# Kernel optimization log

Hardware: AMD Instinct MI355X
Metric: run time of the kernel (lower is better)

Reference implementation:

```python
import jax, jax.numpy as jnp
import numpy as np

DIM = 768
NUM_HEADS = 12
HEAD_DIM = DIM // NUM_HEADS
SCALE = HEAD_DIM ** -0.5
B, N = 4, 2048


def setup_inputs() -> dict:
    key = jax.random.key(0)
    k1, k2, k3 = jax.random.split(key, 3)
    x = jax.random.normal(k1, (B, N, DIM), dtype=jnp.float32)
    W_qk = jax.random.normal(k2, (2 * DIM, DIM), dtype=jnp.float32) * (DIM ** -0.5)
    b_qk = jax.random.normal(k3, (2 * DIM,), dtype=jnp.float32) * 0.02
    return {"x": x, "W_qk": W_qk, "b_qk": b_qk}


def reference(x, W_qk, b_qk):
    Bb, Nn, C = x.shape
    # qk projection: [B,N,2C] -> [B,N,2,H,D] -> q,k each [B,H,N,D]
    qk = x @ W_qk.T + b_qk
    qk = qk.reshape(Bb, Nn, 2, NUM_HEADS, HEAD_DIM).transpose(2, 0, 3, 1, 4)
    q, k = qk[0], qk[1]
    # attention scores [B,H,N,N]
    attn = jnp.einsum("bhnd,bhmd->bhnm", q, k) * SCALE
    attn = jax.nn.softmax(attn, axis=-1)
    # mean over heads, then per-query diagonal -> [B,N]
    attn_weights = jnp.diagonal(attn.mean(axis=1), axis1=-2, axis2=-1)
    return attn_weights
```

## Files before the change

kernel.cpp:

```cpp
#include <hip/hip_runtime.h>
#include <math.h>


#define B_ 4
#define N_ 2048
#define H_ 12
#define D_ 64
#define C_ 768
#define TWO_C 1536
#define QSCALE 0.18033688011112043f

typedef _Float16 half8 __attribute__((ext_vector_type(8)));
typedef _Float16 half4 __attribute__((ext_vector_type(4)));
typedef float floatx4 __attribute__((ext_vector_type(4)));

#if __has_builtin(__builtin_amdgcn_exp2f)
#define EXP2(x) __builtin_amdgcn_exp2f(x)
#else
#define EXP2(x) exp2f(x)
#endif

__device__ __forceinline__ void gload_lds16(const _Float16* g, _Float16* l) {
  __builtin_amdgcn_global_load_lds(
      (const __attribute__((address_space(1))) void*)g,
      (__attribute__((address_space(3))) void*)l, 16, 0, 0);
}

#define NX4 1572864
#define NW4 294912
__global__ __launch_bounds__(256) void conv_kernel(const float* __restrict__ x,
                                                   const float* __restrict__ W,
                                                   _Float16* __restrict__ xh,
                                                   _Float16* __restrict__ wh) {
  int i = blockIdx.x * 256 + threadIdx.x;
  const float* in;
  _Float16* out;
  int idx;
  if (i < NX4) {
    in = x; out = xh; idx = i;
  } else if (i < NX4 + NW4) {
    in = W; out = wh; idx = i - NX4;
  } else {
    return;
  }
  float4 v = ((const float4*)in)[idx];
  half4 o;
  o[0] = (_Float16)v.x; o[1] = (_Float16)v.y;
  o[2] = (_Float16)v.z; o[3] = (_Float16)v.w;
  ((half4*)out)[idx] = o;
}

__global__ __launch_bounds__(256) void proj_kernel(
    const _Float16* __restrict__ xh, const _Float16* __restrict__ wh,
    const float* __restrict__ bias, _Float16* __restrict__ qh,
    _Float16* __restrict__ kh) {
  __shared__ _Float16 As[3][128 * 32];
  __shared__ _Float16 Bs[3][128 * 32];
  const int t = threadIdx.x;
  const int l = t & 63;
  const int w = t >> 6;
  const int wr = w >> 1, wc = w & 1;

  int lin = blockIdx.y * 12 + blockIdx.x;
  int swz = (lin & 7) * 96 + (lin >> 3);
  const int bm = (swz / 12) * 128;
  const int bc = (swz % 12) * 128;

  const int srow = l >> 2;
  const int schunk = (l & 3) ^ ((l >> 3) & 3);

  floatx4 acc[4][4] = {};

#define PSTAGE(KT)                                                          \
  {                                                                         \
    const int sl_ = (KT) % 3;                                               \
    const int k0_ = (KT) * 32;                                              \
    _Pragma("unroll") for (int i_ = 0; i_ < 2; ++i_) {                      \
      int rb_ = w * 32 + i_ * 16;                                           \
      gload_lds16(xh + (size_t)(bm + rb_ + srow) * C_ + k0_ + schunk * 8,   \
                  As[sl_] + rb_ * 32);                                      \
      gload_lds16(wh + (size_t)(bc + rb_ + srow) * C_ + k0_ + schunk * 8,   \
                  Bs[sl_] + rb_ * 32);                                      \
    }                                                                       \
  }

#define PITER(KT, VMASM, DO_STAGE)                                          \
  {                                                                         \
    asm volatile(VMASM ::: "memory");                                       \
    __builtin_amdgcn_s_barrier();                                           \
    asm volatile("" ::: "memory");                                          \
    const int sl_ = (KT) % 3;                                               \
    const _Float16* Ap_ = As[sl_];                                          \
    const _Float16* Bp_ = Bs[sl_];                                          \
    half8 af[4], bf[4];                                                     \
    _Pragma("unroll") for (int fr = 0; fr < 4; ++fr) {                      \
      int row = wr * 64 + fr * 16 + (l & 15);                               \
      int ch = (l >> 4) ^ ((row >> 1) & 3);                                 \
      af[fr] = *(const half8*)(Ap_ + row * 32 + ch * 8);                    \
    }                                                                       \
    _Pragma("unroll") for (int fc = 0; fc < 4; ++fc) {                      \
      int row = wc * 64 + fc * 16 + (l & 15);                               \
      int ch = (l >> 4) ^ ((row >> 1) & 3);                                 \
      bf[fc] = *(const half8*)(Bp_ + row * 32 + ch * 8);                    \
    }                                                                       \
    if (DO_STAGE) PSTAGE((KT) + 2);                                         \
    _Pragma("unroll") for (int fr = 0; fr < 4; ++fr)                        \
        _Pragma("unroll") for (int fc = 0; fc < 4; ++fc) acc[fr][fc] =      \
        __builtin_amdgcn_mfma_f32_16x16x32_f16(af[fr], bf[fc],              \
                                               acc[fr][fc], 0, 0, 0);       \
  }

  PSTAGE(0);
  PSTAGE(1);
  for (int kt = 0; kt < 22; ++kt) PITER(kt, "s_waitcnt vmcnt(4)", true);
  PITER(22, "s_waitcnt vmcnt(4)", false);
  PITER(23, "s_waitcnt vmcnt(0)", false);
#undef PITER
#undef PSTAGE

#pragma unroll
  for (int fr = 0; fr < 4; ++fr) {
#pragma unroll
    for (int fc = 0; fc < 4; ++fc) {
#pragma unroll
      for (int j = 0; j < 4; ++j) {
        int m = bm + wr * 64 + fr * 16 + ((l >> 4) << 2) + j;
        int c = bc + wc * 64 + fc * 16 + (l & 15);
        float v = acc[fr][fc][j] + bias[c];
        int b = m >> 11, n = m & (N_ - 1);
        int cc = (c < C_) ? c : c - C_;
        if (c < C_) v *= QSCALE;
        int hh = cc >> 6, d = cc & 63;
        _Float16* dst = (c < C_) ? qh : kh;
        dst[((((size_t)b * H_ + hh) * N_ + n) << 6) + d] = (_Float16)v;
      }
    }
  }
}

__global__ __launch_bounds__(256) void attn_kernel(
    const _Float16* __restrict__ qh, const _Float16* __restrict__ kh,
    float* __restrict__ part) {
  __shared__ _Float16 ks[4][64 * 64];
  const int t = threadIdx.x;
  const int l = t & 63;
  const int w = t >> 6;

  int lin = blockIdx.x;
  int swz = (lin & 7) * 192 + (lin >> 3);
  const int qt = swz & 31;
  const int h = (swz >> 5) % 12;
  const int b = swz / 384;

  const _Float16* qb = qh + (((size_t)(b * H_ + h) * N_ + qt * 64) << 6);
  const _Float16* kb = kh + (((size_t)(b * H_ + h) * N_) << 6);

  half8 qf[4][2];
#pragma unroll
  for (int fr = 0; fr < 4; ++fr)
#pragma unroll
    for (int kd = 0; kd < 2; ++kd)
      qf[fr][kd] = *(const half8*)(qb + (size_t)(fr * 16 + (l & 15)) * 64 +
                                   kd * 32 + (l >> 4) * 8);

  const int lin0 = w * 64 + l;
  const int row0 = lin0 >> 3, slot0 = lin0 & 7;
  const int soff0 = row0 * 64 + (slot0 ^ (row0 & 7)) * 8;
  const int lin1 = lin0 + 256;
  const int row1 = lin1 >> 3, slot1 = lin1 & 7;
  const int soff1 = row1 * 64 + (slot1 ^ (row1 & 7)) * 8;

#define STAGE(KT)                                                   \
  {                                                                 \
    const _Float16* kp_ = kb + (size_t)(KT) * 4096;                 \
    _Float16* ld_ = ks[(KT) & 3];                                   \
    gload_lds16(kp_ + soff0, ld_ + w * 512);                        \
    gload_lds16(kp_ + soff1, ld_ + w * 512 + 2048);                 \
  }

  const int frow = w * 16 + (l & 15);
  const int koff0 = frow * 64 + (((l >> 4) + 0) ^ (l & 7)) * 8;
  const int koff1 = frow * 64 + (((l >> 4) + 4) ^ (l & 7)) * 8;

  float lsum[4][4] = {};
  float ed[4] = {0.f, 0.f, 0.f, 0.f};
  const floatx4 kZero = {0.f, 0.f, 0.f, 0.f};
  floatx4 accA[4], accB[4];

#define FINB(KT, ACC)                                                         \
  {                                                                           \
    _Pragma("unroll") for (int fr = 0; fr < 4; ++fr)                          \
        _Pragma("unroll") for (int j = 0; j < 4; ++j)                         \
            lsum[fr][j] += EXP2(ACC[fr][j]);                                  \
    if ((KT) == qt) {                                                         \
      _Pragma("unroll") for (int fr = 0; fr < 4; ++fr)                        \
          _Pragma("unroll") for (int j = 0; j < 4; ++j) {                     \
        if (fr == w && (l & 15) == (((l >> 4) << 2) + j))                     \
          ed[j] = EXP2(ACC[fr][j]);                                           \
      }                                                                       \
    }                                                                         \
  }

#define STEP(KT, ACCC, ACCP, VMASM, DO_STAGE, DO_FIN)                         \
  {                                                                           \
    asm volatile(VMASM ::: "memory");                                         \
    __builtin_amdgcn_s_barrier();                                             \
    asm volatile("" ::: "memory");                                            \
    const _Float16* bufp = ks[(KT) & 3];                                      \
    half8 kf0 = *(const half8*)(bufp + koff0);                                \
    half8 kf1 = *(const half8*)(bufp + koff1);                                \
    if (DO_STAGE) STAGE((KT) + 3);                                            \
    if (DO_FIN) FINB((KT) - 1, ACCP);                                         \
    _Pragma("unroll") for (int fr = 0; fr < 4; ++fr) {                        \
      ACCC[fr] = kZero;                                                       \
      ACCC[fr] = __builtin_amdgcn_mfma_f32_16x16x32_f16(qf[fr][0], kf0,       \
                                                        ACCC[fr], 0, 0, 0);   \
      ACCC[fr] = __builtin_amdgcn_mfma_f32_16x16x32_f16(qf[fr][1], kf1,       \
                                                        ACCC[fr], 0, 0, 0);   \
    }                                                                         \
  }

  STAGE(0);
  STAGE(1);
  STAGE(2);

  STEP(0, accA, accB, "s_waitcnt vmcnt(4)", true, false);
  for (int kt = 1; kt < 28; kt += 2) {
    STEP(kt, accB, accA, "s_waitcnt vmcnt(4)", true, true);
    STEP(kt + 1, accA, accB, "s_waitcnt vmcnt(4)", true, true);
  }
  STEP(29, accB, accA, "s_waitcnt vmcnt(4)", false, true);
  STEP(30, accA, accB, "s_waitcnt vmcnt(2)", false, true);
  STEP(31, accB, accA, "s_waitcnt vmcnt(0)", false, true);
  FINB(31, accB);
#undef STEP
#undef FINB
#undef STAGE

#pragma unroll
  for (int fr = 0; fr < 4; ++fr)
#pragma unroll
    for (int j = 0; j < 4; ++j)
#pragma unroll
      for (int m = 1; m < 16; m <<= 1)
        lsum[fr][j] += __shfl_xor(lsum[fr][j], m, 16);
#pragma unroll
  for (int j = 0; j < 4; ++j)
#pragma unroll
    for (int m = 1; m < 16; m <<= 1) ed[j] += __shfl_xor(ed[j], m, 16);

  __builtin_amdgcn_s_barrier();
  float* red = (float*)ks[0];
  float* edl = red + 256;
  if ((l & 15) == 0) {
#pragma unroll
    for (int fr = 0; fr < 4; ++fr)
#pragma unroll
      for (int j = 0; j < 4; ++j)
        red[w * 64 + fr * 16 + ((l >> 4) << 2) + j] = lsum[fr][j];
#pragma unroll
    for (int j = 0; j < 4; ++j) edl[w * 16 + ((l >> 4) << 2) + j] = ed[j];
  }
  __syncthreads();

  if (t < 64) {
    float ls = red[t] + red[64 + t] + red[128 + t] + red[192 + t];
    part[(size_t)(b * H_ + h) * N_ + qt * 64 + t] = edl[t] / ls;
  }
}

__global__ __launch_bounds__(256) void reduce_kernel(
    const float* __restrict__ part, float* __restrict__ out) {
  int g = blockIdx.x * 256 + threadIdx.x;
  if (g >= B_ * N_) return;
  int b = g >> 11, n = g & (N_ - 1);
  float s = 0.0f;
#pragma unroll
  for (int hh = 0; hh < H_; ++hh) s += part[(size_t)(b * H_ + hh) * N_ + n];
  out[g] = s * (1.0f / (float)H_);
}

extern "C" void kernel_launch(void* const* d_in, const int* in_sizes, int n_in,
                              void* d_out, int out_size, void* d_ws,
                              size_t ws_size, hipStream_t stream) {
  const float* x = (const float*)d_in[0];
  const float* W = (const float*)d_in[1];
  const float* bias = (const float*)d_in[2];
  float* out = (float*)d_out;

  char* ws = (char*)d_ws;
  _Float16* xh = (_Float16*)ws;
  _Float16* wh = (_Float16*)(ws + 12582912);
  _Float16* qh = (_Float16*)(ws + 14942208);
  _Float16* kh = (_Float16*)(ws + 27525120);
  float* part = (float*)(ws + 40108032);

  conv_kernel<<<(NX4 + NW4 + 255) / 256, 256, 0, stream>>>(x, W, xh, wh);
  proj_kernel<<<dim3(TWO_C / 128, 8192 / 128), 256, 0, stream>>>(xh, wh, bias,
                                                                 qh, kh);
  attn_kernel<<<N_ / 64 * H_ * B_, 256, 0, stream>>>(qh, kh, part);
  reduce_kernel<<<(B_ * N_ + 255) / 256, 256, 0, stream>>>(part, out);
}
```

Baseline: 84.45 us.

## Double query tile per block to 128 rows and drop accumulator double-buffering

Each attention block now processes 128 query rows (8 MFMA fragments) instead of 64, so every staged K tile in LDS is reused across twice as many queries and total K traffic halves. The grid shrinks to 768 blocks. The software-pipelined accA/accB ping-pong that overlapped exp with the next tile's MFMAs is replaced by a single accumulator computed and exponentiated in the same iteration. This costs more registers, which may lower occupancy, and leaves less overlap between MFMA and exp work.

Result: no change. 84.91 us (+0.5%).

```diff
diff --git a/kernel.cpp b/kernel.cpp
--- a/kernel.cpp
+++ b/kernel.cpp
@@ -147,17 +147,17 @@
   const int w = t >> 6;
 
   int lin = blockIdx.x;
-  int swz = (lin & 7) * 192 + (lin >> 3);
-  const int qt = swz & 31;
-  const int h = (swz >> 5) % 12;
-  const int b = swz / 384;
-
-  const _Float16* qb = qh + (((size_t)(b * H_ + h) * N_ + qt * 64) << 6);
+  int swz = (lin & 7) * 96 + (lin >> 3);
+  const int qt = swz & 15;
+  const int h = (swz >> 4) % 12;
+  const int b = swz / 192;
+
+  const _Float16* qb = qh + (((size_t)(b * H_ + h) * N_ + qt * 128) << 6);
   const _Float16* kb = kh + (((size_t)(b * H_ + h) * N_) << 6);
 
-  half8 qf[4][2];
-#pragma unroll
-  for (int fr = 0; fr < 4; ++fr)
+  half8 qf[8][2];
+#pragma unroll
+  for (int fr = 0; fr < 8; ++fr)
 #pragma unroll
     for (int kd = 0; kd < 2; ++kd)
       qf[fr][kd] = *(const half8*)(qb + (size_t)(fr * 16 + (l & 15)) * 64 +
@@ -182,26 +182,15 @@
   const int koff0 = frow * 64 + (((l >> 4) + 0) ^ (l & 7)) * 8;
   const int koff1 = frow * 64 + (((l >> 4) + 4) ^ (l & 7)) * 8;
 
-  float lsum[4][4] = {};
-  float ed[4] = {0.f, 0.f, 0.f, 0.f};
-  const floatx4 kZero = {0.f, 0.f, 0.f, 0.f};
-  floatx4 accA[4], accB[4];
-
-#define FINB(KT, ACC)                                                         \
-  {                                                                           \
-    _Pragma("unroll") for (int fr = 0; fr < 4; ++fr)                          \
-        _Pragma("unroll") for (int j = 0; j < 4; ++j)                         \
-            lsum[fr][j] += EXP2(ACC[fr][j]);                                  \
-    if ((KT) == qt) {                                                         \
-      _Pragma("unroll") for (int fr = 0; fr < 4; ++fr)                        \
-          _Pragma("unroll") for (int j = 0; j < 4; ++j) {                     \
-        if (fr == w && (l & 15) == (((l >> 4) << 2) + j))                     \
-          ed[j] = EXP2(ACC[fr][j]);                                           \
-      }                                                                       \
-    }                                                                         \
-  }
-
-#define STEP(KT, ACCC, ACCP, VMASM, DO_STAGE, DO_FIN)                         \
+  float lsum[8][4] = {};
+  float ed0[4] = {0.f, 0.f, 0.f, 0.f};
+  float ed1[4] = {0.f, 0.f, 0.f, 0.f};
+
+  STAGE(0);
+  STAGE(1);
+  STAGE(2);
+
+#define ITER(KT, VMASM, DO_STAGE)                                             \
   {                                                                           \
     asm volatile(VMASM ::: "memory");                                         \
     __builtin_amdgcn_s_barrier();                                             \
@@ -210,35 +199,41 @@
     half8 kf0 = *(const half8*)(bufp + koff0);                                \
     half8 kf1 = *(const half8*)(bufp + koff1);                                \
     if (DO_STAGE) STAGE((KT) + 3);                                            \
-    if (DO_FIN) FINB((KT) - 1, ACCP);                                         \
-    _Pragma("unroll") for (int fr = 0; fr < 4; ++fr) {                        \
-      ACCC[fr] = kZero;                                                       \
-      ACCC[fr] = __builtin_amdgcn_mfma_f32_16x16x32_f16(qf[fr][0], kf0,       \
-                                                        ACCC[fr], 0, 0, 0);   \
-      ACCC[fr] = __builtin_amdgcn_mfma_f32_16x16x32_f16(qf[fr][1], kf1,       \
-                                                        ACCC[fr], 0, 0, 0);   \
+    floatx4 acc[8] = {};                                                      \
+    _Pragma("unroll") for (int fr = 0; fr < 8; ++fr) {                        \
+      acc[fr] = __builtin_amdgcn_mfma_f32_16x16x32_f16(qf[fr][0], kf0,        \
+                                                       acc[fr], 0, 0, 0);     \
+      acc[fr] = __builtin_amdgcn_mfma_f32_16x16x32_f16(qf[fr][1], kf1,        \
+                                                       acc[fr], 0, 0, 0);     \
     }                                                                         \
-  }
-
-  STAGE(0);
-  STAGE(1);
-  STAGE(2);
-
-  STEP(0, accA, accB, "s_waitcnt vmcnt(4)", true, false);
-  for (int kt = 1; kt < 28; kt += 2) {
-    STEP(kt, accB, accA, "s_waitcnt vmcnt(4)", true, true);
-    STEP(kt + 1, accA, accB, "s_waitcnt vmcnt(4)", true, true);
-  }
-  STEP(29, accB, accA, "s_waitcnt vmcnt(4)", false, true);
-  STEP(30, accA, accB, "s_waitcnt vmcnt(2)", false, true);
-  STEP(31, accB, accA, "s_waitcnt vmcnt(0)", false, true);
-  FINB(31, accB);
-#undef STEP
-#undef FINB
+    _Pragma("unroll") for (int fr = 0; fr < 8; ++fr)                          \
+        _Pragma("unroll") for (int j = 0; j < 4; ++j)                         \
+            lsum[fr][j] += EXP2(acc[fr][j]);                                  \
+    if ((KT) == 2 * qt) {                                                     \
+      _Pragma("unroll") for (int fr = 0; fr < 8; ++fr)                        \
+          _Pragma("unroll") for (int j = 0; j < 4; ++j) {                     \
+        if (fr == w && (l & 15) == (((l >> 4) << 2) + j))                     \
+          ed0[j] = EXP2(acc[fr][j]);                                          \
+      }                                                                       \
+    }                                                                         \
+    if ((KT) == 2 * qt + 1) {                                                 \
+      _Pragma("unroll") for (int fr = 0; fr < 8; ++fr)                        \
+          _Pragma("unroll") for (int j = 0; j < 4; ++j) {                     \
+        if (fr == w + 4 && (l & 15) == (((l >> 4) << 2) + j))                 \
+          ed1[j] = EXP2(acc[fr][j]);                                          \
+      }                                                                       \
+    }                                                                         \
+  }
+
+  for (int kt = 0; kt < 29; ++kt) ITER(kt, "s_waitcnt vmcnt(4)", true);
+  ITER(29, "s_waitcnt vmcnt(4)", false);
+  ITER(30, "s_waitcnt vmcnt(2)", false);
+  ITER(31, "s_waitcnt vmcnt(0)", false);
+#undef ITER
 #undef STAGE
 
 #pragma unroll
-  for (int fr = 0; fr < 4; ++fr)
+  for (int fr = 0; fr < 8; ++fr)
 #pragma unroll
     for (int j = 0; j < 4; ++j)
 #pragma unroll
@@ -247,25 +242,31 @@
 #pragma unroll
   for (int j = 0; j < 4; ++j)
 #pragma unroll
-    for (int m = 1; m < 16; m <<= 1) ed[j] += __shfl_xor(ed[j], m, 16);
+    for (int m = 1; m < 16; m <<= 1) {
+      ed0[j] += __shfl_xor(ed0[j], m, 16);
+      ed1[j] += __shfl_xor(ed1[j], m, 16);
+    }
 
   __builtin_amdgcn_s_barrier();
   float* red = (float*)ks[0];
-  float* edl = red + 256;
+  float* edl = red + 512;
   if ((l & 15) == 0) {
 #pragma unroll
-    for (int fr = 0; fr < 4; ++fr)
+    for (int fr = 0; fr < 8; ++fr)
 #pragma unroll
       for (int j = 0; j < 4; ++j)
-        red[w * 64 + fr * 16 + ((l >> 4) << 2) + j] = lsum[fr][j];
-#pragma unroll
-    for (int j = 0; j < 4; ++j) edl[w * 16 + ((l >> 4) << 2) + j] = ed[j];
+        red[w * 128 + fr * 16 + ((l >> 4) << 2) + j] = lsum[fr][j];
+#pragma unroll
+    for (int j = 0; j < 4; ++j) {
+      edl[w * 16 + ((l >> 4) << 2) + j] = ed0[j];
+      edl[64 + w * 16 + ((l >> 4) << 2) + j] = ed1[j];
+    }
   }
   __syncthreads();
 
-  if (t < 64) {
-    float ls = red[t] + red[64 + t] + red[128 + t] + red[192 + t];
-    part[(size_t)(b * H_ + h) * N_ + qt * 64 + t] = edl[t] / ls;
+  if (t < 128) {
+    float ls = red[t] + red[128 + t] + red[256 + t] + red[384 + t];
+    part[(size_t)(b * H_ + h) * N_ + qt * 128 + t] = edl[t] / ls;
   }
 }
 
@@ -298,6 +299,6 @@
   conv_kernel<<<(NX4 + NW4 + 255) / 256, 256, 0, stream>>>(x, W, xh, wh);
   proj_kernel<<<dim3(TWO_C / 128, 8192 / 128), 256, 0, stream>>>(xh, wh, bias,
                                                                  qh, kh);
-  attn_kernel<<<N_ / 64 * H_ * B_, 256, 0, stream>>>(qh, kh, part);
+  attn_kernel<<<N_ / 128 * H_ * B_, 256, 0, stream>>>(qh, kh, part);
   reduce_kernel<<<(B_ * N_ + 255) / 256, 256, 0, stream>>>(part, out);
 }
```

## Process K tiles in pairs and fuse head reduction via atomics

Applied to the files above, without the earlier changes.

The attention loop now stages and consumes two 64-key tiles per iteration, using a 3-slot buffer of 128-key pairs in place of a 4-slot ring of single tiles. Both accumulator sets are computed and their exponentials summed in the same iteration, which halves the number of barriers. The separate reduce kernel is removed: the output is zeroed inside the conversion kernel and each attention block adds its head's contribution with atomicAdd. This saves one launch and the round trip through the partial buffer, at the cost of atomic contention and a summation order that is no longer deterministic.

Measured after the change: 126.9 us. 50.2% more time.

```diff
diff --git a/kernel.cpp b/kernel.cpp
--- a/kernel.cpp
+++ b/kernel.cpp
@@ -31,8 +31,13 @@
 __global__ __launch_bounds__(256) void conv_kernel(const float* __restrict__ x,
                                                    const float* __restrict__ W,
                                                    _Float16* __restrict__ xh,
-                                                   _Float16* __restrict__ wh) {
+                                                   _Float16* __restrict__ wh,
+                                                   float* __restrict__ outz) {
   int i = blockIdx.x * 256 + threadIdx.x;
+  if (i < 2048) {
+    float4 z; z.x = 0.f; z.y = 0.f; z.z = 0.f; z.w = 0.f;
+    ((float4*)outz)[i] = z;
+  }
   const float* in;
   _Float16* out;
   int idx;
@@ -140,8 +145,8 @@
 
 __global__ __launch_bounds__(256) void attn_kernel(
     const _Float16* __restrict__ qh, const _Float16* __restrict__ kh,
-    float* __restrict__ part) {
-  __shared__ _Float16 ks[4][64 * 64];
+    float* __restrict__ out) {
+  __shared__ _Float16 ks[3 * 8192];
   const int t = threadIdx.x;
   const int l = t & 63;
   const int w = t >> 6;
@@ -170,12 +175,14 @@
   const int row1 = lin1 >> 3, slot1 = lin1 & 7;
   const int soff1 = row1 * 64 + (slot1 ^ (row1 & 7)) * 8;
 
-#define STAGE(KT)                                                   \
+#define SPAIR(PM, SLOT)                                             \
   {                                                                 \
-    const _Float16* kp_ = kb + (size_t)(KT) * 4096;                 \
-    _Float16* ld_ = ks[(KT) & 3];                                   \
+    const _Float16* kp_ = kb + (size_t)(PM) * 8192;                 \
+    _Float16* ld_ = ks + (SLOT) * 8192;                             \
     gload_lds16(kp_ + soff0, ld_ + w * 512);                        \
     gload_lds16(kp_ + soff1, ld_ + w * 512 + 2048);                 \
+    gload_lds16(kp_ + 4096 + soff0, ld_ + 4096 + w * 512);          \
+    gload_lds16(kp_ + 4096 + soff1, ld_ + 4096 + w * 512 + 2048);   \
   }
 
   const int frow = w * 16 + (l & 15);
@@ -184,58 +191,65 @@
 
   float lsum[4][4] = {};
   float ed[4] = {0.f, 0.f, 0.f, 0.f};
-  const floatx4 kZero = {0.f, 0.f, 0.f, 0.f};
-  floatx4 accA[4], accB[4];
-
-#define FINB(KT, ACC)                                                         \
+
+#define DIAG(ACC)                                                             \
   {                                                                           \
     _Pragma("unroll") for (int fr = 0; fr < 4; ++fr)                          \
-        _Pragma("unroll") for (int j = 0; j < 4; ++j)                         \
-            lsum[fr][j] += EXP2(ACC[fr][j]);                                  \
-    if ((KT) == qt) {                                                         \
-      _Pragma("unroll") for (int fr = 0; fr < 4; ++fr)                        \
-          _Pragma("unroll") for (int j = 0; j < 4; ++j) {                     \
-        if (fr == w && (l & 15) == (((l >> 4) << 2) + j))                     \
-          ed[j] = EXP2(ACC[fr][j]);                                           \
-      }                                                                       \
+        _Pragma("unroll") for (int j = 0; j < 4; ++j) {                       \
+      if (fr == w && (l & 15) == (((l >> 4) << 2) + j))                       \
+        ed[j] = EXP2(ACC[fr][j]);                                             \
     }                                                                         \
   }
 
-#define STEP(KT, ACCC, ACCP, VMASM, DO_STAGE, DO_FIN)                         \
+#define ITER(PM, SLOT, VMASM, SPM, SSLOT, DO_STAGE)                           \
   {                                                                           \
     asm volatile(VMASM ::: "memory");                                         \
     __builtin_amdgcn_s_barrier();                                             \
     asm volatile("" ::: "memory");                                            \
-    const _Float16* bufp = ks[(KT) & 3];                                      \
-    half8 kf0 = *(const half8*)(bufp + koff0);                                \
-    half8 kf1 = *(const half8*)(bufp + koff1);                                \
-    if (DO_STAGE) STAGE((KT) + 3);                                            \
-    if (DO_FIN) FINB((KT) - 1, ACCP);                                         \
+    const _Float16* base_ = ks + (SLOT) * 8192;                               \
+    half8 kfA0 = *(const half8*)(base_ + koff0);                              \
+    half8 kfA1 = *(const half8*)(base_ + koff1);                              \
+    half8 kfB0 = *(const half8*)(base_ + 4096 + koff0);                       \
+    half8 kfB1 = *(const half8*)(base_ + 4096 + koff1);                       \
+    if (DO_STAGE) SPAIR(SPM, SSLOT);                                          \
+    floatx4 accA[4] = {};                                                     \
+    floatx4 accB[4] = {};                                                     \
     _Pragma("unroll") for (int fr = 0; fr < 4; ++fr) {                        \
-      ACCC[fr] = kZero;                                                       \
-      ACCC[fr] = __builtin_amdgcn_mfma_f32_16x16x32_f16(qf[fr][0], kf0,       \
-                                                        ACCC[fr], 0, 0, 0);   \
-      ACCC[fr] = __builtin_amdgcn_mfma_f32_16x16x32_f16(qf[fr][1], kf1,       \
-                                                        ACCC[fr], 0, 0, 0);   \
+      accA[fr] = __builtin_amdgcn_mfma_f32_16x16x32_f16(qf[fr][0], kfA0,      \
+                                                        accA[fr], 0, 0, 0);   \
+      accA[fr] = __builtin_amdgcn_mfma_f32_16x16x32_f16(qf[fr][1], kfA1,      \
+                                                        accA[fr], 0, 0, 0);   \
     }                                                                         \
-  }
-
-  STAGE(0);
-  STAGE(1);
-  STAGE(2);
-
-  STEP(0, accA, accB, "s_waitcnt vmcnt(4)", true, false);
-  for (int kt = 1; kt < 28; kt += 2) {
-    STEP(kt, accB, accA, "s_waitcnt vmcnt(4)", true, true);
-    STEP(kt + 1, accA, accB, "s_waitcnt vmcnt(4)", true, true);
-  }
-  STEP(29, accB, accA, "s_waitcnt vmcnt(4)", false, true);
-  STEP(30, accA, accB, "s_waitcnt vmcnt(2)", false, true);
-  STEP(31, accB, accA, "s_waitcnt vmcnt(0)", false, true);
-  FINB(31, accB);
-#undef STEP
-#undef FINB
-#undef STAGE
+    _Pragma("unroll") for (int fr = 0; fr < 4; ++fr) {                        \
+      accB[fr] = __builtin_amdgcn_mfma_f32_16x16x32_f16(qf[fr][0], kfB0,      \
+                                                        accB[fr], 0, 0, 0);   \
+      accB[fr] = __builtin_amdgcn_mfma_f32_16x16x32_f16(qf[fr][1], kfB1,      \
+                                                        accB[fr], 0, 0, 0);   \
+    }                                                                         \
+    _Pragma("unroll") for (int fr = 0; fr < 4; ++fr)                          \
+        _Pragma("unroll") for (int j = 0; j < 4; ++j)                         \
+            lsum[fr][j] += EXP2(accA[fr][j]) + EXP2(accB[fr][j]);             \
+    if (2 * (PM) == qt) DIAG(accA);                                           \
+    if (2 * (PM) + 1 == qt) DIAG(accB);                                       \
+  }
+
+  SPAIR(0, 0);
+  SPAIR(1, 1);
+
+#pragma unroll
+  for (int m = 0; m < 4; ++m) {
+    int pm = m * 3;
+    ITER(pm + 0, 0, "s_waitcnt vmcnt(4)", pm + 2, 2, true);
+    ITER(pm + 1, 1, "s_waitcnt vmcnt(4)", pm + 3, 0, true);
+    ITER(pm + 2, 2, "s_waitcnt vmcnt(4)", pm + 4, 1, true);
+  }
+  ITER(12, 0, "s_waitcnt vmcnt(4)", 14, 2, true);
+  ITER(13, 1, "s_waitcnt vmcnt(4)", 15, 0, true);
+  ITER(14, 2, "s_waitcnt vmcnt(4)", 0, 0, false);
+  ITER(15, 0, "s_waitcnt vmcnt(0)", 0, 0, false);
+#undef ITER
+#undef DIAG
+#undef SPAIR
 
 #pragma unroll
   for (int fr = 0; fr < 4; ++fr)
@@ -250,7 +264,7 @@
     for (int m = 1; m < 16; m <<= 1) ed[j] += __shfl_xor(ed[j], m, 16);
 
   __builtin_amdgcn_s_barrier();
-  float* red = (float*)ks[0];
+  float* red = (float*)ks;
   float* edl = red + 256;
   if ((l & 15) == 0) {
 #pragma unroll
@@ -265,19 +279,9 @@
 
   if (t < 64) {
     float ls = red[t] + red[64 + t] + red[128 + t] + red[192 + t];
-    part[(size_t)(b * H_ + h) * N_ + qt * 64 + t] = edl[t] / ls;
-  }
-}
-
-__global__ __launch_bounds__(256) void reduce_kernel(
-    const float* __restrict__ part, float* __restrict__ out) {
-  int g = blockIdx.x * 256 + threadIdx.x;
-  if (g >= B_ * N_) return;
-  int b = g >> 11, n = g & (N_ - 1);
-  float s = 0.0f;
-#pragma unroll
-  for (int hh = 0; hh < H_; ++hh) s += part[(size_t)(b * H_ + hh) * N_ + n];
-  out[g] = s * (1.0f / (float)H_);
+    atomicAdd(out + (size_t)b * N_ + qt * 64 + t,
+              edl[t] / ls * (1.0f / (float)H_));
+  }
 }
 
 extern "C" void kernel_launch(void* const* d_in, const int* in_sizes, int n_in,
@@ -293,11 +297,9 @@
   _Float16* wh = (_Float16*)(ws + 12582912);
   _Float16* qh = (_Float16*)(ws + 14942208);
   _Float16* kh = (_Float16*)(ws + 27525120);
-  float* part = (float*)(ws + 40108032);
-
-  conv_kernel<<<(NX4 + NW4 + 255) / 256, 256, 0, stream>>>(x, W, xh, wh);
+
+  conv_kernel<<<(NX4 + NW4 + 255) / 256, 256, 0, stream>>>(x, W, xh, wh, out);
   proj_kernel<<<dim3(TWO_C / 128, 8192 / 128), 256, 0, stream>>>(xh, wh, bias,
                                                                  qh, kh);
-  attn_kernel<<<N_ / 64 * H_ * B_, 256, 0, stream>>>(qh, kh, part);
-  reduce_kernel<<<(B_ * N_ + 255) / 256, 256, 0, stream>>>(part, out);
-}
+  attn_kernel<<<N_ / 64 * H_ * B_, 256, 0, stream>>>(qh, kh, out);
+}
```
